# Optimization experiments

Measured on AMD Instinct MI355X. Metric: run time of the kernel, lower is better.

## Reference

```python
import jax, jax.numpy as jnp
import numpy as np

NEG_INF = -1.0e9


def setup_inputs() -> dict:
    key = jax.random.key(0)
    ks = jax.random.split(key, 8)
    B, H, S, D = 8, 8, 1024, 64
    return {
        "gv_feat": jax.random.normal(ks[0], (B, D), dtype=jnp.float32),
        "query2": jax.random.normal(ks[1], (B, H, S, D), dtype=jnp.float32),
        "key": jax.random.normal(ks[2], (B, H, S, D), dtype=jnp.float32),
        "att_mask": jax.random.randint(ks[3], (B, S), 0, 2, dtype=jnp.int32),
        "value1": jax.random.normal(ks[4], (B, H, S, D), dtype=jnp.float32),
        "value2": jax.random.normal(ks[5], (B, H, S, D), dtype=jnp.float32),
        "W_ch": jax.random.normal(ks[6], (D, D), dtype=jnp.float32) * (1.0 / np.sqrt(D)),
        "b_ch": jnp.zeros((D,), dtype=jnp.float32),
    }


def reference(gv_feat, query2, key, att_mask, value1, value2, W_ch, b_ch):
    # query2/key/value1/value2: [B, H, S, D]; att_mask: [B, S]
    D = query2.shape[-1]
    scaling = D ** (-0.5)
    # spatial attention: masked scaled QK^T softmax
    scores = jnp.einsum("bhqd,bhkd->bhqk", query2, key) * scaling  # [B,H,S,S]
    mask = att_mask[:, None, None, :]  # [B,1,1,S]
    scores = jnp.where(mask == 0, NEG_INF, scores)
    alpha_spatial = jax.nn.softmax(scores, axis=-1)
    attn2 = jnp.einsum("bhqk,bhkd->bhqd", alpha_spatial, value2)  # [B,H,S,D]
    # channel attention: sigmoid-gated linear over elementwise value1*key
    att_map_channel = value1 * key  # [B,H,S,D]
    alpha_channel = jax.nn.sigmoid(
        jnp.einsum("bhsd,ed->bhse", att_map_channel, W_ch) + b_ch
    )
    attn2 = alpha_channel * attn2
    return (gv_feat, attn2)
```

## Files before the change

### kernel.cpp

```cpp
#include <hip/hip_runtime.h>
#include <hip/hip_bf16.h>

typedef __attribute__((ext_vector_type(4)))  float f32x4;
typedef __attribute__((ext_vector_type(16))) float f32x16;
typedef __attribute__((ext_vector_type(8)))  short bf16x8;
typedef __attribute__((ext_vector_type(4)))  unsigned u32x4;
typedef __attribute__((ext_vector_type(2)))  unsigned u32x2;

#define NEG_INF_F (-1000000000.0f)

__device__ inline unsigned pkbf(float a, float b) {
    union { __hip_bfloat16 h; unsigned short u; } x, y;
    x.h = __float2bfloat16(a);
    y.h = __float2bfloat16(b);
    return (unsigned)x.u | ((unsigned)y.u << 16);
}

__global__ __launch_bounds__(512) void aoa_attn_kernel(
    const float* __restrict__ gv,
    const float* __restrict__ q2,
    const float* __restrict__ keyp,
    const int*   __restrict__ maskp,
    const float* __restrict__ v1,
    const float* __restrict__ v2,
    const float* __restrict__ W,
    const float* __restrict__ bch,
    float* __restrict__ out)
{
    constexpr int S = 1024, D = 64;
    const int bh  = blockIdx.x;
    const int qt  = blockIdx.y;
    const int b   = bh >> 3;
    const int tid = threadIdx.x;
    const int wid = tid >> 6;
    const int lane = tid & 63;
    const int l31 = lane & 31;
    const int h   = lane >> 5;

    float* out_attn = out + 512;
    if (bh == 0 && qt == 0) out[tid] = gv[tid];

    __shared__ float maskf[S];
    __shared__ short Klds[2][64][72];
    __shared__ short Vt[2][64][72];
    __shared__ float Lw[8][32];

    for (int i = tid; i < S; i += 512)
        maskf[i] = maskp[b * S + i] ? 0.0f : NEG_INF_F;

    const size_t base = (size_t)bh * S * D;
    const float* Qp  = q2   + base;
    const float* Kp  = keyp + base;
    const float* V1p = v1   + base;
    const float* V2p = v2   + base;

    const int q0   = qt * 256 + wid * 32;
    const int qrow = q0 + l31;

    bf16x8 bq[4];
    #pragma unroll
    for (int ds = 0; ds < 4; ++ds) {
        const f32x4* p = (const f32x4*)(Qp + (size_t)qrow * D + ds * 16 + h * 8);
        f32x4 x0 = p[0], x1 = p[1];
        u32x4 u = (u32x4){pkbf(x0[0], x0[1]), pkbf(x0[2], x0[3]),
                          pkbf(x1[0], x1[1]), pkbf(x1[2], x1[3])};
        bq[ds] = *(bf16x8*)&u;
    }

    f32x16 acc_o[2];
    #pragma unroll
    for (int dh = 0; dh < 2; ++dh)
        #pragma unroll
        for (int r = 0; r < 16; ++r) acc_o[dh][r] = 0.0f;

    float m_run = -1e30f, l_run = 0.0f;
    const float SC = 0.125f * 1.4426950408889634f;

    const int kk   = tid >> 3;
    const int d0   = (tid & 7) << 3;
    const int dcol = tid & 63;
    const int kr0  = (tid >> 6) << 3;

    f32x4 kA, kB;
    float vv[8];
    {
        const f32x4* src = (const f32x4*)(Kp + (size_t)kk * D + d0);
        kA = src[0]; kB = src[1];
        #pragma unroll
        for (int i = 0; i < 8; ++i) vv[i] = V2p[(size_t)(kr0 + i) * D + dcol];
    }
    *(u32x4*)&Klds[0][kk][d0] = (u32x4){pkbf(kA[0], kA[1]), pkbf(kA[2], kA[3]),
                                        pkbf(kB[0], kB[1]), pkbf(kB[2], kB[3])};
    *(u32x4*)&Vt[0][dcol][kr0] = (u32x4){pkbf(vv[0], vv[1]), pkbf(vv[2], vv[3]),
                                         pkbf(vv[4], vv[5]), pkbf(vv[6], vv[7])};
    int cur = 0;

    for (int t = 0; t < 16; ++t) {
        const int kt = t * 64;
        __syncthreads();

        if (t < 15) {
            const f32x4* src = (const f32x4*)(Kp + (size_t)(kt + 64 + kk) * D + d0);
            kA = src[0]; kB = src[1];
            #pragma unroll
            for (int i = 0; i < 8; ++i) vv[i] = V2p[(size_t)(kt + 64 + kr0 + i) * D + dcol];
        }

        f32x16 a0;
        #pragma unroll
        for (int r = 0; r < 16; ++r) a0[r] = 0.0f;
        #pragma unroll
        for (int ds = 0; ds < 4; ++ds) {
            bf16x8 ak = *(const bf16x8*)&Klds[cur][l31][ds * 16 + h * 8];
            a0 = __builtin_amdgcn_mfma_f32_32x32x16_bf16(ak, bq[ds], a0, 0, 0, 0);
        }
        f32x16 a1;
        #pragma unroll
        for (int r = 0; r < 16; ++r) a1[r] = 0.0f;
        #pragma unroll
        for (int ds = 0; ds < 4; ++ds) {
            bf16x8 ak = *(const bf16x8*)&Klds[cur][32 + l31][ds * 16 + h * 8];
            a1 = __builtin_amdgcn_mfma_f32_32x32x16_bf16(ak, bq[ds], a1, 0, 0, 0);
        }

        unsigned w0[8];
        {
            float s[16];
            float tmax = -1e30f;
            #pragma unroll
            for (int g = 0; g < 4; ++g) {
                f32x4 mk = *(const f32x4*)&maskf[kt + g * 8 + h * 4];
                #pragma unroll
                for (int j = 0; j < 4; ++j) {
                    float val = fmaf(a0[g * 4 + j], SC, mk[j]);
                    s[g * 4 + j] = val;
                    tmax = fmaxf(tmax, val);
                }
            }
            tmax = fmaxf(tmax, __shfl_xor(tmax, 32));
            if (__any(tmax > m_run + 8.0f)) {
                float mnew = fmaxf(m_run, tmax);
                float r = __builtin_amdgcn_exp2f(m_run - mnew);
                l_run *= r;
                #pragma unroll
                for (int dh = 0; dh < 2; ++dh)
                    #pragma unroll
                    for (int r2 = 0; r2 < 16; ++r2) acc_o[dh][r2] *= r;
                m_run = mnew;
            }
            float ps0 = 0.f, ps1 = 0.f;
            #pragma unroll
            for (int i = 0; i < 8; ++i) {
                float p0 = __builtin_amdgcn_exp2f(s[2 * i]     - m_run);
                float p1 = __builtin_amdgcn_exp2f(s[2 * i + 1] - m_run);
                ps0 += p0; ps1 += p1;
                w0[i] = pkbf(p0, p1);
            }
            float psum = ps0 + ps1;
            psum += __shfl_xor(psum, 32);
            l_run += psum;
        }

        #pragma unroll
        for (int t2 = 0; t2 < 2; ++t2) {
            u32x2 r0 = __builtin_amdgcn_permlane32_swap(w0[t2 * 4 + 0], w0[t2 * 4 + 2], false, false);
            u32x2 r1 = __builtin_amdgcn_permlane32_swap(w0[t2 * 4 + 1], w0[t2 * 4 + 3], false, false);
            u32x4 ua = (u32x4){r0[0], r1[0], r0[1], r1[1]};
            bf16x8 pa = *(bf16x8*)&ua;
            #pragma unroll
            for (int dh = 0; dh < 2; ++dh) {
                bf16x8 bv = *(const bf16x8*)&Vt[cur][dh * 32 + l31][t2 * 16 + h * 8];
                acc_o[dh] = __builtin_amdgcn_mfma_f32_32x32x16_bf16(pa, bv, acc_o[dh], 0, 0, 0);
            }
        }

        unsigned w1[8];
        {
            float s[16];
            float tmax = -1e30f;
            #pragma unroll
            for (int g = 0; g < 4; ++g) {
                f32x4 mk = *(const f32x4*)&maskf[kt + 32 + g * 8 + h * 4];
                #pragma unroll
                for (int j = 0; j < 4; ++j) {
                    float val = fmaf(a1[g * 4 + j], SC, mk[j]);
                    s[g * 4 + j] = val;
                    tmax = fmaxf(tmax, val);
                }
            }
            tmax = fmaxf(tmax, __shfl_xor(tmax, 32));
            if (__any(tmax > m_run + 8.0f)) {
                float mnew = fmaxf(m_run, tmax);
                float r = __builtin_amdgcn_exp2f(m_run - mnew);
                l_run *= r;
                #pragma unroll
                for (int dh = 0; dh < 2; ++dh)
                    #pragma unroll
                    for (int r2 = 0; r2 < 16; ++r2) acc_o[dh][r2] *= r;
                m_run = mnew;
            }
            float ps0 = 0.f, ps1 = 0.f;
            #pragma unroll
            for (int i = 0; i < 8; ++i) {
                float p0 = __builtin_amdgcn_exp2f(s[2 * i]     - m_run);
                float p1 = __builtin_amdgcn_exp2f(s[2 * i + 1] - m_run);
                ps0 += p0; ps1 += p1;
                w1[i] = pkbf(p0, p1);
            }
            float psum = ps0 + ps1;
            psum += __shfl_xor(psum, 32);
            l_run += psum;
        }

        #pragma unroll
        for (int t2 = 0; t2 < 2; ++t2) {
            u32x2 r0 = __builtin_amdgcn_permlane32_swap(w1[t2 * 4 + 0], w1[t2 * 4 + 2], false, false);
            u32x2 r1 = __builtin_amdgcn_permlane32_swap(w1[t2 * 4 + 1], w1[t2 * 4 + 3], false, false);
            u32x4 ua = (u32x4){r0[0], r1[0], r0[1], r1[1]};
            bf16x8 pa = *(bf16x8*)&ua;
            #pragma unroll
            for (int dh = 0; dh < 2; ++dh) {
                bf16x8 bv = *(const bf16x8*)&Vt[cur][dh * 32 + l31][32 + t2 * 16 + h * 8];
                acc_o[dh] = __builtin_amdgcn_mfma_f32_32x32x16_bf16(pa, bv, acc_o[dh], 0, 0, 0);
            }
        }

        if (t < 15) {
            *(u32x4*)&Klds[cur ^ 1][kk][d0] = (u32x4){pkbf(kA[0], kA[1]), pkbf(kA[2], kA[3]),
                                                      pkbf(kB[0], kB[1]), pkbf(kB[2], kB[3])};
            *(u32x4*)&Vt[cur ^ 1][dcol][kr0] = (u32x4){pkbf(vv[0], vv[1]), pkbf(vv[2], vv[3]),
                                                       pkbf(vv[4], vv[5]), pkbf(vv[6], vv[7])};
        }
        cur ^= 1;
    }

    f32x16 acc_g[2];
    #pragma unroll
    for (int eh = 0; eh < 2; ++eh)
        #pragma unroll
        for (int r = 0; r < 16; ++r) acc_g[eh][r] = 0.0f;

    bf16x8 bam[4];
    #pragma unroll
    for (int ds = 0; ds < 4; ++ds) {
        const f32x4* p1 = (const f32x4*)(V1p + (size_t)qrow * D + ds * 16 + h * 8);
        const f32x4* pk = (const f32x4*)(Kp  + (size_t)qrow * D + ds * 16 + h * 8);
        f32x4 a0 = p1[0], a1 = p1[1], c0 = pk[0], c1 = pk[1];
        u32x4 u = (u32x4){pkbf(a0[0] * c0[0], a0[1] * c0[1]), pkbf(a0[2] * c0[2], a0[3] * c0[3]),
                          pkbf(a1[0] * c1[0], a1[1] * c1[1]), pkbf(a1[2] * c1[2], a1[3] * c1[3])};
        bam[ds] = *(bf16x8*)&u;
    }
    #pragma unroll
    for (int eh = 0; eh < 2; ++eh) {
        #pragma unroll
        for (int ds = 0; ds < 4; ++ds) {
            const f32x4* pw = (const f32x4*)(W + (size_t)(eh * 32 + l31) * D + ds * 16 + h * 8);
            f32x4 x0 = pw[0], x1 = pw[1];
            u32x4 u = (u32x4){pkbf(x0[0], x0[1]), pkbf(x0[2], x0[3]),
                              pkbf(x1[0], x1[1]), pkbf(x1[2], x1[3])};
            bf16x8 bw = *(bf16x8*)&u;
            acc_g[eh] = __builtin_amdgcn_mfma_f32_32x32x16_bf16(bam[ds], bw, acc_g[eh], 0, 0, 0);
        }
    }

    Lw[wid][l31] = 1.0f / l_run;
    __builtin_amdgcn_wave_barrier();
    const float bv0 = bch[l31], bv1 = bch[32 + l31];
    #pragma unroll
    for (int dh = 0; dh < 2; ++dh) {
        const float bc = dh ? bv1 : bv0;
        #pragma unroll
        for (int r = 0; r < 16; ++r) {
            const int ql = (r & 3) + 8 * (r >> 2) + 4 * h;
            float invl = Lw[wid][ql];
            float o = acc_o[dh][r] * invl;
            float z = acc_g[dh][r] + bc;
            float gate = 1.0f / (1.0f + __expf(-z));
            out_attn[base + (size_t)(q0 + ql) * D + dh * 32 + l31] = o * gate;
        }
    }
}

extern "C" void kernel_launch(void* const* d_in, const int* in_sizes, int n_in,
                              void* d_out, int out_size, void* d_ws, size_t ws_size,
                              hipStream_t stream) {
    const float* gv   = (const float*)d_in[0];
    const float* q2   = (const float*)d_in[1];
    const float* keyp = (const float*)d_in[2];
    const int*   mask = (const int*)  d_in[3];
    const float* v1   = (const float*)d_in[4];
    const float* v2   = (const float*)d_in[5];
    const float* W    = (const float*)d_in[6];
    const float* bch  = (const float*)d_in[7];
    float* out = (float*)d_out;

    dim3 grid(64, 4);
    aoa_attn_kernel<<<grid, 512, 0, stream>>>(gv, q2, keyp, mask, v1, v2, W, bch, out);
}
```

Baseline: 46.93 us.

## Split KV range across two blocks and merge partial softmax results in combine kernel

```diff
diff --git a/kernel.cpp b/kernel.cpp
--- a/kernel.cpp
+++ b/kernel.cpp
@@ -1,6 +1,7 @@
 #include <hip/hip_runtime.h>
 #include <hip/hip_bf16.h>
 
+typedef __attribute__((ext_vector_type(2)))  float f32x2;
 typedef __attribute__((ext_vector_type(4)))  float f32x4;
 typedef __attribute__((ext_vector_type(16))) float f32x16;
 typedef __attribute__((ext_vector_type(8)))  short bf16x8;
@@ -25,11 +26,14 @@
     const float* __restrict__ v2,
     const float* __restrict__ W,
     const float* __restrict__ bch,
-    float* __restrict__ out)
+    float* __restrict__ out,
+    int kvlen, int nsplit,
+    float* __restrict__ ga, float* __restrict__ ml)
 {
     constexpr int S = 1024, D = 64;
-    const int bh  = blockIdx.x;
-    const int qt  = blockIdx.y;
+    const int bh    = blockIdx.x;
+    const int qt    = blockIdx.y;
+    const int split = blockIdx.z;
     const int b   = bh >> 3;
     const int tid = threadIdx.x;
     const int wid = tid >> 6;
@@ -38,7 +42,7 @@
     const int h   = lane >> 5;
 
     float* out_attn = out + 512;
-    if (bh == 0 && qt == 0) out[tid] = gv[tid];
+    if (bh == 0 && qt == 0 && split == 0) out[tid] = gv[tid];
 
     __shared__ float maskf[S];
     __shared__ short Klds[2][64][72];
@@ -56,6 +60,8 @@
 
     const int q0   = qt * 256 + wid * 32;
     const int qrow = q0 + l31;
+    const int kv0  = split * kvlen;
+    const int NT   = kvlen >> 6;
 
     bf16x8 bq[4];
     #pragma unroll
@@ -84,10 +90,10 @@
     f32x4 kA, kB;
     float vv[8];
     {
-        const f32x4* src = (const f32x4*)(Kp + (size_t)kk * D + d0);
+        const f32x4* src = (const f32x4*)(Kp + (size_t)(kv0 + kk) * D + d0);
         kA = src[0]; kB = src[1];
         #pragma unroll
-        for (int i = 0; i < 8; ++i) vv[i] = V2p[(size_t)(kr0 + i) * D + dcol];
+        for (int i = 0; i < 8; ++i) vv[i] = V2p[(size_t)(kv0 + kr0 + i) * D + dcol];
     }
     *(u32x4*)&Klds[0][kk][d0] = (u32x4){pkbf(kA[0], kA[1]), pkbf(kA[2], kA[3]),
                                         pkbf(kB[0], kB[1]), pkbf(kB[2], kB[3])};
@@ -95,11 +101,11 @@
                                          pkbf(vv[4], vv[5]), pkbf(vv[6], vv[7])};
     int cur = 0;
 
-    for (int t = 0; t < 16; ++t) {
-        const int kt = t * 64;
+    for (int t = 0; t < NT; ++t) {
+        const int kt = kv0 + t * 64;
         __syncthreads();
 
-        if (t < 15) {
+        if (t < NT - 1) {
             const f32x4* src = (const f32x4*)(Kp + (size_t)(kt + 64 + kk) * D + d0);
             kA = src[0]; kB = src[1];
             #pragma unroll
@@ -225,7 +231,7 @@
             }
         }
 
-        if (t < 15) {
+        if (t < NT - 1) {
             *(u32x4*)&Klds[cur ^ 1][kk][d0] = (u32x4){pkbf(kA[0], kA[1]), pkbf(kA[2], kA[3]),
                                                       pkbf(kB[0], kB[1]), pkbf(kB[2], kB[3])};
             *(u32x4*)&Vt[cur ^ 1][dcol][kr0] = (u32x4){pkbf(vv[0], vv[1]), pkbf(vv[2], vv[3]),
@@ -263,21 +269,65 @@
         }
     }
 
-    Lw[wid][l31] = 1.0f / l_run;
-    __builtin_amdgcn_wave_barrier();
     const float bv0 = bch[l31], bv1 = bch[32 + l31];
-    #pragma unroll
-    for (int dh = 0; dh < 2; ++dh) {
-        const float bc = dh ? bv1 : bv0;
-        #pragma unroll
-        for (int r = 0; r < 16; ++r) {
-            const int ql = (r & 3) + 8 * (r >> 2) + 4 * h;
-            float invl = Lw[wid][ql];
-            float o = acc_o[dh][r] * invl;
-            float z = acc_g[dh][r] + bc;
-            float gate = 1.0f / (1.0f + __expf(-z));
-            out_attn[base + (size_t)(q0 + ql) * D + dh * 32 + l31] = o * gate;
-        }
+
+    if (nsplit == 1) {
+        Lw[wid][l31] = 1.0f / l_run;
+        __builtin_amdgcn_wave_barrier();
+        #pragma unroll
+        for (int dh = 0; dh < 2; ++dh) {
+            const float bc = dh ? bv1 : bv0;
+            #pragma unroll
+            for (int r = 0; r < 16; ++r) {
+                const int ql = (r & 3) + 8 * (r >> 2) + 4 * h;
+                float invl = Lw[wid][ql];
+                float o = acc_o[dh][r] * invl;
+                float z = acc_g[dh][r] + bc;
+                float gate = 1.0f / (1.0f + __expf(-z));
+                out_attn[base + (size_t)(q0 + ql) * D + dh * 32 + l31] = o * gate;
+            }
+        }
+    } else {
+        const size_t rbase = (size_t)(split * 64 + bh) * S;
+        if (h == 0) {
+            size_t mi = (rbase + qrow) * 2;
+            ml[mi]     = m_run;
+            ml[mi + 1] = l_run;
+        }
+        #pragma unroll
+        for (int dh = 0; dh < 2; ++dh) {
+            const float bc = dh ? bv1 : bv0;
+            #pragma unroll
+            for (int r = 0; r < 16; ++r) {
+                const int ql = (r & 3) + 8 * (r >> 2) + 4 * h;
+                float z = acc_g[dh][r] + bc;
+                float gate = 1.0f / (1.0f + __expf(-z));
+                ga[(rbase + q0 + ql) * 64 + dh * 32 + l31] = acc_o[dh][r] * gate;
+            }
+        }
+    }
+}
+
+__global__ __launch_bounds__(256) void aoa_combine_kernel(
+    const float* __restrict__ ga, const float* __restrict__ ml,
+    float* __restrict__ out_attn)
+{
+    const int tot = 64 * 1024 * 16;
+    for (int i4 = blockIdx.x * 256 + threadIdx.x; i4 < tot; i4 += gridDim.x * 256) {
+        const int row = i4 >> 4;
+        const int dof = (i4 & 15) << 2;
+        f32x2 s0 = *(const f32x2*)&ml[(size_t)row * 2];
+        f32x2 s1 = *(const f32x2*)&ml[(size_t)(65536 + row) * 2];
+        float M  = fmaxf(s0[0], s1[0]);
+        float w1 = __builtin_amdgcn_exp2f(s0[0] - M);
+        float w2 = __builtin_amdgcn_exp2f(s1[0] - M);
+        float inv = 1.0f / (w1 * s0[1] + w2 * s1[1]);
+        f32x4 g1 = *(const f32x4*)&ga[(size_t)row * 64 + dof];
+        f32x4 g2 = *(const f32x4*)&ga[(size_t)(65536 + row) * 64 + dof];
+        f32x4 o;
+        #pragma unroll
+        for (int j = 0; j < 4; ++j) o[j] = (w1 * g1[j] + w2 * g2[j]) * inv;
+        *(f32x4*)&out_attn[(size_t)row * 64 + dof] = o;
     }
 }
 
@@ -294,6 +344,16 @@
     const float* bch  = (const float*)d_in[7];
     float* out = (float*)d_out;
 
-    dim3 grid(64, 4);
-    aoa_attn_kernel<<<grid, 512, 0, stream>>>(gv, q2, keyp, mask, v1, v2, W, bch, out);
+    const size_t GA_ELEMS = 2ull * 64 * 1024 * 64;
+    const size_t ML_ELEMS = 2ull * 64 * 1024 * 2;
+    const size_t need = (GA_ELEMS + ML_ELEMS) * 4;
+    const int nsplit = (ws_size >= need) ? 2 : 1;
+    float* ga = (float*)d_ws;
+    float* ml = ga + GA_ELEMS;
+
+    dim3 grid(64, 4, nsplit);
+    aoa_attn_kernel<<<grid, 512, 0, stream>>>(gv, q2, keyp, mask, v1, v2, W, bch, out,
+                                              1024 / nsplit, nsplit, ga, ml);
+    if (nsplit == 2)
+        aoa_combine_kernel<<<1024, 256, 0, stream>>>(ga, ml, out + 512);
 }
```

Result: slower. 71.24 us (+51.8%).

## Precompute bf16 K and transposed V in prep kernel, read directly from global

Applied to the files above, without the earlier changes.

```diff
diff --git a/kernel.cpp b/kernel.cpp
--- a/kernel.cpp
+++ b/kernel.cpp
@@ -15,16 +15,71 @@
     y.h = __float2bfloat16(b);
     return (unsigned)x.u | ((unsigned)y.u << 16);
 }
-
-__global__ __launch_bounds__(512) void aoa_attn_kernel(
+__device__ inline short bf1(float a) {
+    union { __hip_bfloat16 h; short s; } x; x.h = __float2bfloat16(a); return x.s;
+}
+
+__global__ __launch_bounds__(256) void aoa_prep_kernel(
+    const float* __restrict__ keyp, const float* __restrict__ v2,
+    const int* __restrict__ maskp,
+    short* __restrict__ Kb, short* __restrict__ Vt, float* __restrict__ maskw)
+{
+    const int bh  = blockIdx.x;
+    const int c   = blockIdx.y;
+    const int tid = threadIdx.x;
+    const int kv0 = c * 64;
+    const size_t base = (size_t)bh * 65536;
+
+    __shared__ short T[64][72];
+
+    {
+        const int k    = tid >> 2;
+        const int dseg = (tid & 3) << 4;
+        const f32x4* ks = (const f32x4*)(keyp + base + (size_t)(kv0 + k) * 64 + dseg);
+        f32x4 a0 = ks[0], a1 = ks[1], a2 = ks[2], a3 = ks[3];
+        u32x4 w0 = (u32x4){pkbf(a0[0],a0[1]), pkbf(a0[2],a0[3]), pkbf(a1[0],a1[1]), pkbf(a1[2],a1[3])};
+        u32x4 w1 = (u32x4){pkbf(a2[0],a2[1]), pkbf(a2[2],a2[3]), pkbf(a3[0],a3[1]), pkbf(a3[2],a3[3])};
+        short* kd = Kb + base + (size_t)(kv0 + k) * 64 + dseg;
+        *(u32x4*)kd = w0; *(u32x4*)(kd + 8) = w1;
+
+        const f32x4* vs = (const f32x4*)(v2 + base + (size_t)(kv0 + k) * 64 + dseg);
+        f32x4 b0 = vs[0], b1 = vs[1], b2 = vs[2], b3 = vs[3];
+        u32x4 t0 = (u32x4){pkbf(b0[0],b0[1]), pkbf(b0[2],b0[3]), pkbf(b1[0],b1[1]), pkbf(b1[2],b1[3])};
+        u32x4 t1 = (u32x4){pkbf(b2[0],b2[1]), pkbf(b2[2],b2[3]), pkbf(b3[0],b3[1]), pkbf(b3[2],b3[3])};
+        *(u32x4*)&T[k][dseg]     = t0;
+        *(u32x4*)&T[k][dseg + 8] = t1;
+    }
+    __syncthreads();
+    {
+        const int d    = tid >> 2;
+        const int kseg = (tid & 3) << 4;
+        short tmp[16];
+        #pragma unroll
+        for (int i = 0; i < 16; ++i) tmp[i] = T[kseg + i][d];
+        short* vd = Vt + base + (size_t)d * 1024 + kv0 + kseg;
+        *(u32x4*)vd       = *(u32x4*)&tmp[0];
+        *(u32x4*)(vd + 8) = *(u32x4*)&tmp[8];
+    }
+    if (c == 0 && bh < 8) {
+        #pragma unroll
+        for (int i = 0; i < 4; ++i) {
+            int idx = tid * 4 + i - 3 * tid;
+        }
+        for (int i = tid; i < 1024; i += 256)
+            maskw[bh * 1024 + i] = maskp[bh * 1024 + i] ? 0.0f : NEG_INF_F;
+    }
+}
+
+__global__ __launch_bounds__(256) void aoa_attn_kernel(
     const float* __restrict__ gv,
     const float* __restrict__ q2,
     const float* __restrict__ keyp,
-    const int*   __restrict__ maskp,
     const float* __restrict__ v1,
-    const float* __restrict__ v2,
     const float* __restrict__ W,
     const float* __restrict__ bch,
+    const short* __restrict__ Kb,
+    const short* __restrict__ Vt,
+    const float* __restrict__ maskw,
     float* __restrict__ out)
 {
     constexpr int S = 1024, D = 64;
@@ -32,29 +87,22 @@
     const int qt  = blockIdx.y;
     const int b   = bh >> 3;
     const int tid = threadIdx.x;
+    const int lane = tid & 63;
     const int wid = tid >> 6;
-    const int lane = tid & 63;
     const int l31 = lane & 31;
     const int h   = lane >> 5;
 
     float* out_attn = out + 512;
-    if (bh == 0 && qt == 0) out[tid] = gv[tid];
-
-    __shared__ float maskf[S];
-    __shared__ short Klds[2][64][72];
-    __shared__ short Vt[2][64][72];
-    __shared__ float Lw[8][32];
-
-    for (int i = tid; i < S; i += 512)
-        maskf[i] = maskp[b * S + i] ? 0.0f : NEG_INF_F;
-
-    const size_t base = (size_t)bh * S * D;
-    const float* Qp  = q2   + base;
+    if (bh == 0 && qt == 0) { out[tid] = gv[tid]; out[tid + 256] = gv[tid + 256]; }
+
+    const size_t base  = (size_t)bh * S * D;
+    const size_t bbase = (size_t)bh * 65536;
+    const float* Qp  = q2 + base;
+    const float* V1p = v1 + base;
     const float* Kp  = keyp + base;
-    const float* V1p = v1   + base;
-    const float* V2p = v2   + base;
-
-    const int q0   = qt * 256 + wid * 32;
+    const float* mrow = maskw + b * S;
+
+    const int q0   = qt * 128 + wid * 32;
     const int qrow = q0 + l31;
 
     bf16x8 bq[4];
@@ -76,60 +124,33 @@
     float m_run = -1e30f, l_run = 0.0f;
     const float SC = 0.125f * 1.4426950408889634f;
 
-    const int kk   = tid >> 3;
-    const int d0   = (tid & 7) << 3;
-    const int dcol = tid & 63;
-    const int kr0  = (tid >> 6) << 3;
-
-    f32x4 kA, kB;
-    float vv[8];
-    {
-        const f32x4* src = (const f32x4*)(Kp + (size_t)kk * D + d0);
-        kA = src[0]; kB = src[1];
-        #pragma unroll
-        for (int i = 0; i < 8; ++i) vv[i] = V2p[(size_t)(kr0 + i) * D + dcol];
-    }
-    *(u32x4*)&Klds[0][kk][d0] = (u32x4){pkbf(kA[0], kA[1]), pkbf(kA[2], kA[3]),
-                                        pkbf(kB[0], kB[1]), pkbf(kB[2], kB[3])};
-    *(u32x4*)&Vt[0][dcol][kr0] = (u32x4){pkbf(vv[0], vv[1]), pkbf(vv[2], vv[3]),
-                                         pkbf(vv[4], vv[5]), pkbf(vv[6], vv[7])};
-    int cur = 0;
-
+    const short* Kbase  = Kb + bbase + (size_t)l31 * 64 + h * 8;
+    const short* Vbase  = Vt + bbase + (size_t)l31 * 1024 + h * 8;
+
+    #pragma unroll 2
     for (int t = 0; t < 16; ++t) {
         const int kt = t * 64;
-        __syncthreads();
-
-        if (t < 15) {
-            const f32x4* src = (const f32x4*)(Kp + (size_t)(kt + 64 + kk) * D + d0);
-            kA = src[0]; kB = src[1];
-            #pragma unroll
-            for (int i = 0; i < 8; ++i) vv[i] = V2p[(size_t)(kt + 64 + kr0 + i) * D + dcol];
-        }
-
-        f32x16 a0;
-        #pragma unroll
-        for (int r = 0; r < 16; ++r) a0[r] = 0.0f;
+
+        f32x16 a0, a1;
+        #pragma unroll
+        for (int r = 0; r < 16; ++r) { a0[r] = 0.0f; a1[r] = 0.0f; }
         #pragma unroll
         for (int ds = 0; ds < 4; ++ds) {
-            bf16x8 ak = *(const bf16x8*)&Klds[cur][l31][ds * 16 + h * 8];
+            bf16x8 ak = *(const bf16x8*)(Kbase + (size_t)kt * 64 + ds * 16);
             a0 = __builtin_amdgcn_mfma_f32_32x32x16_bf16(ak, bq[ds], a0, 0, 0, 0);
         }
-        f32x16 a1;
-        #pragma unroll
-        for (int r = 0; r < 16; ++r) a1[r] = 0.0f;
         #pragma unroll
         for (int ds = 0; ds < 4; ++ds) {
-            bf16x8 ak = *(const bf16x8*)&Klds[cur][32 + l31][ds * 16 + h * 8];
+            bf16x8 ak = *(const bf16x8*)(Kbase + (size_t)(kt + 32) * 64 + ds * 16);
             a1 = __builtin_amdgcn_mfma_f32_32x32x16_bf16(ak, bq[ds], a1, 0, 0, 0);
         }
 
         unsigned w0[8];
         {
-            float s[16];
-            float tmax = -1e30f;
+            float s[16], tmax = -1e30f;
             #pragma unroll
             for (int g = 0; g < 4; ++g) {
-                f32x4 mk = *(const f32x4*)&maskf[kt + g * 8 + h * 4];
+                f32x4 mk = *(const f32x4*)&mrow[kt + g * 8 + h * 4];
                 #pragma unroll
                 for (int j = 0; j < 4; ++j) {
                     float val = fmaf(a0[g * 4 + j], SC, mk[j]);
@@ -169,18 +190,17 @@
             bf16x8 pa = *(bf16x8*)&ua;
             #pragma unroll
             for (int dh = 0; dh < 2; ++dh) {
-                bf16x8 bv = *(const bf16x8*)&Vt[cur][dh * 32 + l31][t2 * 16 + h * 8];
+                bf16x8 bv = *(const bf16x8*)(Vbase + (size_t)(dh * 32) * 1024 + kt + t2 * 16);
                 acc_o[dh] = __builtin_amdgcn_mfma_f32_32x32x16_bf16(pa, bv, acc_o[dh], 0, 0, 0);
             }
         }
 
         unsigned w1[8];
         {
-            float s[16];
-            float tmax = -1e30f;
+            float s[16], tmax = -1e30f;
             #pragma unroll
             for (int g = 0; g < 4; ++g) {
-                f32x4 mk = *(const f32x4*)&maskf[kt + 32 + g * 8 + h * 4];
+                f32x4 mk = *(const f32x4*)&mrow[kt + 32 + g * 8 + h * 4];
                 #pragma unroll
                 for (int j = 0; j < 4; ++j) {
                     float val = fmaf(a1[g * 4 + j], SC, mk[j]);
@@ -220,18 +240,10 @@
             bf16x8 pa = *(bf16x8*)&ua;
             #pragma unroll
             for (int dh = 0; dh < 2; ++dh) {
-                bf16x8 bv = *(const bf16x8*)&Vt[cur][dh * 32 + l31][32 + t2 * 16 + h * 8];
+                bf16x8 bv = *(const bf16x8*)(Vbase + (size_t)(dh * 32) * 1024 + kt + 32 + t2 * 16);
                 acc_o[dh] = __builtin_amdgcn_mfma_f32_32x32x16_bf16(pa, bv, acc_o[dh], 0, 0, 0);
             }
         }
-
-        if (t < 15) {
-            *(u32x4*)&Klds[cur ^ 1][kk][d0] = (u32x4){pkbf(kA[0], kA[1]), pkbf(kA[2], kA[3]),
-                                                      pkbf(kB[0], kB[1]), pkbf(kB[2], kB[3])};
-            *(u32x4*)&Vt[cur ^ 1][dcol][kr0] = (u32x4){pkbf(vv[0], vv[1]), pkbf(vv[2], vv[3]),
-                                                       pkbf(vv[4], vv[5]), pkbf(vv[6], vv[7])};
-        }
-        cur ^= 1;
     }
 
     f32x16 acc_g[2];
@@ -246,8 +258,8 @@
         const f32x4* p1 = (const f32x4*)(V1p + (size_t)qrow * D + ds * 16 + h * 8);
         const f32x4* pk = (const f32x4*)(Kp  + (size_t)qrow * D + ds * 16 + h * 8);
         f32x4 a0 = p1[0], a1 = p1[1], c0 = pk[0], c1 = pk[1];
-        u32x4 u = (u32x4){pkbf(a0[0] * c0[0], a0[1] * c0[1]), pkbf(a0[2] * c0[2], a0[3] * c0[3]),
-                          pkbf(a1[0] * c1[0], a1[1] * c1[1]), pkbf(a1[2] * c1[2], a1[3] * c1[3])};
+        u32x4 u = (u32x4){pkbf(a0[0]*c0[0], a0[1]*c0[1]), pkbf(a0[2]*c0[2], a0[3]*c0[3]),
+                          pkbf(a1[0]*c1[0], a1[1]*c1[1]), pkbf(a1[2]*c1[2], a1[3]*c1[3])};
         bam[ds] = *(bf16x8*)&u;
     }
     #pragma unroll
@@ -263,8 +275,7 @@
         }
     }
 
-    Lw[wid][l31] = 1.0f / l_run;
-    __builtin_amdgcn_wave_barrier();
+    float inv = 1.0f / l_run;
     const float bv0 = bch[l31], bv1 = bch[32 + l31];
     #pragma unroll
     for (int dh = 0; dh < 2; ++dh) {
@@ -272,7 +283,7 @@
         #pragma unroll
         for (int r = 0; r < 16; ++r) {
             const int ql = (r & 3) + 8 * (r >> 2) + 4 * h;
-            float invl = Lw[wid][ql];
+            float invl = __shfl(inv, ql);
             float o = acc_o[dh][r] * invl;
             float z = acc_g[dh][r] + bc;
             float gate = 1.0f / (1.0f + __expf(-z));
@@ -294,6 +305,13 @@
     const float* bch  = (const float*)d_in[7];
     float* out = (float*)d_out;
 
-    dim3 grid(64, 4);
-    aoa_attn_kernel<<<grid, 512, 0, stream>>>(gv, q2, keyp, mask, v1, v2, W, bch, out);
-}
+    short* Kb    = (short*)d_ws;
+    short* Vt    = Kb + 64ull * 1024 * 64;
+    float* maskw = (float*)(Vt + 64ull * 1024 * 64);
+
+    dim3 pgrid(64, 16);
+    aoa_prep_kernel<<<pgrid, 256, 0, stream>>>(keyp, v2, mask, Kb, Vt, maskw);
+
+    dim3 agrid(64, 8);
+    aoa_attn_kernel<<<agrid, 256, 0, stream>>>(gv, q2, keyp, v1, W, bch, Kb, Vt, maskw, out);
+}
```

Measured after the change: 96.17 us. 2.05x slower.

## Compact valid keys per batch and skip fully masked key tiles

Applied to the files above, without the earlier changes.

```diff
diff --git a/kernel.cpp b/kernel.cpp
--- a/kernel.cpp
+++ b/kernel.cpp
@@ -16,15 +16,47 @@
     return (unsigned)x.u | ((unsigned)y.u << 16);
 }
 
+__global__ __launch_bounds__(1024) void aoa_prep_kernel(
+    const int* __restrict__ maskp,
+    int* __restrict__ vidx, float* __restrict__ padmask, int* __restrict__ nvalid)
+{
+    const int b   = blockIdx.x;
+    const int tid = threadIdx.x;
+    const int lane = tid & 63;
+
+    const int m = maskp[b * 1024 + tid] ? 1 : 0;
+    unsigned long long bal = __ballot(m);
+    const int wpre = __popcll(bal & ((1ull << lane) - 1ull));
+
+    __shared__ int wsum[16], woff[16];
+    if (lane == 63) wsum[tid >> 6] = wpre + m;
+    __syncthreads();
+    if (tid < 16) {
+        int off = 0;
+        for (int i = 0; i < tid; ++i) off += wsum[i];
+        woff[tid] = off;
+    }
+    __syncthreads();
+    const int pos = woff[tid >> 6] + wpre;
+    const int nv  = woff[15] + wsum[15];
+
+    if (m) vidx[b * 1024 + pos] = tid;
+    if (tid >= nv) vidx[b * 1024 + tid] = 0;
+    padmask[b * 1024 + tid] = (tid < nv) ? 0.0f : NEG_INF_F;
+    if (tid == 0) nvalid[b] = nv;
+}
+
 __global__ __launch_bounds__(512) void aoa_attn_kernel(
     const float* __restrict__ gv,
     const float* __restrict__ q2,
     const float* __restrict__ keyp,
-    const int*   __restrict__ maskp,
     const float* __restrict__ v1,
     const float* __restrict__ v2,
     const float* __restrict__ W,
     const float* __restrict__ bch,
+    const int*   __restrict__ vidx,
+    const float* __restrict__ padmask,
+    const int*   __restrict__ nvalid,
     float* __restrict__ out)
 {
     constexpr int S = 1024, D = 64;
@@ -40,13 +72,19 @@
     float* out_attn = out + 512;
     if (bh == 0 && qt == 0) out[tid] = gv[tid];
 
-    __shared__ float maskf[S];
+    __shared__ float pmL[S];
+    __shared__ int   vidxL[S];
     __shared__ short Klds[2][64][72];
     __shared__ short Vt[2][64][72];
     __shared__ float Lw[8][32];
 
-    for (int i = tid; i < S; i += 512)
-        maskf[i] = maskp[b * S + i] ? 0.0f : NEG_INF_F;
+    for (int i = tid; i < S; i += 512) {
+        pmL[i]   = padmask[b * S + i];
+        vidxL[i] = vidx[b * S + i];
+    }
+
+    const int nv = nvalid[b];
+    const int NT = (nv + 63) >> 6;
 
     const size_t base = (size_t)bh * S * D;
     const float* Qp  = q2   + base;
@@ -81,13 +119,15 @@
     const int dcol = tid & 63;
     const int kr0  = (tid >> 6) << 3;
 
+    __syncthreads();
+
     f32x4 kA, kB;
     float vv[8];
     {
-        const f32x4* src = (const f32x4*)(Kp + (size_t)kk * D + d0);
+        const f32x4* src = (const f32x4*)(Kp + (size_t)vidxL[kk] * D + d0);
         kA = src[0]; kB = src[1];
         #pragma unroll
-        for (int i = 0; i < 8; ++i) vv[i] = V2p[(size_t)(kr0 + i) * D + dcol];
+        for (int i = 0; i < 8; ++i) vv[i] = V2p[(size_t)vidxL[kr0 + i] * D + dcol];
     }
     *(u32x4*)&Klds[0][kk][d0] = (u32x4){pkbf(kA[0], kA[1]), pkbf(kA[2], kA[3]),
                                         pkbf(kB[0], kB[1]), pkbf(kB[2], kB[3])};
@@ -95,15 +135,15 @@
                                          pkbf(vv[4], vv[5]), pkbf(vv[6], vv[7])};
     int cur = 0;
 
-    for (int t = 0; t < 16; ++t) {
+    for (int t = 0; t < NT; ++t) {
         const int kt = t * 64;
         __syncthreads();
 
-        if (t < 15) {
-            const f32x4* src = (const f32x4*)(Kp + (size_t)(kt + 64 + kk) * D + d0);
+        if (t < NT - 1) {
+            const f32x4* src = (const f32x4*)(Kp + (size_t)vidxL[kt + 64 + kk] * D + d0);
             kA = src[0]; kB = src[1];
             #pragma unroll
-            for (int i = 0; i < 8; ++i) vv[i] = V2p[(size_t)(kt + 64 + kr0 + i) * D + dcol];
+            for (int i = 0; i < 8; ++i) vv[i] = V2p[(size_t)vidxL[kt + 64 + kr0 + i] * D + dcol];
         }
 
         f32x16 a0;
@@ -125,11 +165,10 @@
 
         unsigned w0[8];
         {
-            float s[16];
-            float tmax = -1e30f;
+            float s[16], tmax = -1e30f;
             #pragma unroll
             for (int g = 0; g < 4; ++g) {
-                f32x4 mk = *(const f32x4*)&maskf[kt + g * 8 + h * 4];
+                f32x4 mk = *(const f32x4*)&pmL[kt + g * 8 + h * 4];
                 #pragma unroll
                 for (int j = 0; j < 4; ++j) {
                     float val = fmaf(a0[g * 4 + j], SC, mk[j]);
@@ -176,11 +215,10 @@
 
         unsigned w1[8];
         {
-            float s[16];
-            float tmax = -1e30f;
+            float s[16], tmax = -1e30f;
             #pragma unroll
             for (int g = 0; g < 4; ++g) {
-                f32x4 mk = *(const f32x4*)&maskf[kt + 32 + g * 8 + h * 4];
+                f32x4 mk = *(const f32x4*)&pmL[kt + 32 + g * 8 + h * 4];
                 #pragma unroll
                 for (int j = 0; j < 4; ++j) {
                     float val = fmaf(a1[g * 4 + j], SC, mk[j]);
@@ -225,7 +263,7 @@
             }
         }
 
-        if (t < 15) {
+        if (t < NT - 1) {
             *(u32x4*)&Klds[cur ^ 1][kk][d0] = (u32x4){pkbf(kA[0], kA[1]), pkbf(kA[2], kA[3]),
                                                       pkbf(kB[0], kB[1]), pkbf(kB[2], kB[3])};
             *(u32x4*)&Vt[cur ^ 1][dcol][kr0] = (u32x4){pkbf(vv[0], vv[1]), pkbf(vv[2], vv[3]),
@@ -246,8 +284,8 @@
         const f32x4* p1 = (const f32x4*)(V1p + (size_t)qrow * D + ds * 16 + h * 8);
         const f32x4* pk = (const f32x4*)(Kp  + (size_t)qrow * D + ds * 16 + h * 8);
         f32x4 a0 = p1[0], a1 = p1[1], c0 = pk[0], c1 = pk[1];
-        u32x4 u = (u32x4){pkbf(a0[0] * c0[0], a0[1] * c0[1]), pkbf(a0[2] * c0[2], a0[3] * c0[3]),
-                          pkbf(a1[0] * c1[0], a1[1] * c1[1]), pkbf(a1[2] * c1[2], a1[3] * c1[3])};
+        u32x4 u = (u32x4){pkbf(a0[0]*c0[0], a0[1]*c0[1]), pkbf(a0[2]*c0[2], a0[3]*c0[3]),
+                          pkbf(a1[0]*c1[0], a1[1]*c1[1]), pkbf(a1[2]*c1[2], a1[3]*c1[3])};
         bam[ds] = *(bf16x8*)&u;
     }
     #pragma unroll
@@ -294,6 +332,13 @@
     const float* bch  = (const float*)d_in[7];
     float* out = (float*)d_out;
 
+    int*   vidx    = (int*)d_ws;
+    float* padmask = (float*)(vidx + 8 * 1024);
+    int*   nvalid  = (int*)(padmask + 8 * 1024);
+
+    aoa_prep_kernel<<<8, 1024, 0, stream>>>(mask, vidx, padmask, nvalid);
+
     dim3 grid(64, 4);
-    aoa_attn_kernel<<<grid, 512, 0, stream>>>(gv, q2, keyp, mask, v1, v2, W, bch, out);
+    aoa_attn_kernel<<<grid, 512, 0, stream>>>(gv, q2, keyp, v1, v2, W, bch,
+                                              vidx, padmask, nvalid, out);
 }
```

New measurement: 41.36 us, median of 2. -11.9%, faster.
